# Performance work log

Hardware: AMD Instinct MI355X
Metric: run time of the kernel (lower is better)

Reference implementation:

```python
import jax, jax.numpy as jnp
import numpy as np

N_S, N_T = 64, 32
N_EFF = N_S * N_T          # 2048
K_T1, K_T2 = 8, 8
BATCH = 16


def _orthonormal(key, n):
    q, _ = jnp.linalg.qr(jax.random.normal(key, (n, n), dtype=jnp.float32))
    return q.astype(jnp.float32)


def setup_inputs() -> dict:
    key = jax.random.key(0)
    ks = jax.random.split(key, 6)
    return {
        "s_effective_batch": jax.random.normal(ks[0], (BATCH, N_EFF), dtype=jnp.float32),
        "U_G": _orthonormal(ks[1], N_S),
        "U_P_T": _orthonormal(ks[2], N_T),
        "h0": jax.random.normal(ks[3], (N_EFF,), dtype=jnp.float32) * 0.01,
        "h_hat_1_coeffs": jax.random.normal(ks[4], (N_S, K_T1), dtype=jnp.float32) * 0.01,
        "H_hat_2_S": jax.random.normal(ks[5], (N_S, N_S), dtype=jnp.float32) * 0.01,
        "H_hat_2_T_coeffs": jax.random.normal(jax.random.fold_in(key, 7), (K_T2, K_T2), dtype=jnp.float32) * 0.01,
    }


def reference(s_effective_batch, U_G, U_P_T, h0, h_hat_1_coeffs, H_hat_2_S, H_hat_2_T_coeffs):
    # spatio-temporal basis via Kronecker product: [N_eff, N_eff]
    U_ST = jnp.kron(U_G, U_P_T)

    # GFT as in the module: s_hat = s @ U_ST
    s_hat = s_effective_batch @ U_ST                       # [B, N_eff]

    # linear (first-order Volterra) term
    Ub1 = U_P_T[:, :K_T1]                                  # [N_T, K1]
    full_h_hat_1 = (h_hat_1_coeffs @ Ub1.T).reshape(-1)    # [N_eff]
    z1 = (full_h_hat_1[None, :] * s_hat) @ U_ST            # iGFT as in module: @ U_ST

    # quadratic kernel H2 = kron(H2_S, Ub2 @ C @ Ub2^T)
    Ub2 = U_P_T[:, :K_T2]
    full_H2_T = Ub2 @ (H_hat_2_T_coeffs @ Ub2.T)           # [N_T, N_T]
    H2 = jnp.kron(H_hat_2_S, full_H2_T)                    # [N_eff, N_eff]

    # z2[b,i] = diag( U_ST (H2 * s_hat_b s_hat_b^T) U_ST^T )_i
    #         = sum_{k,l} B[b,i,k] H2[k,l] B[b,i,l], with B[b,i,k] = U_ST[i,k]*s_hat[b,k]
    B = U_ST[None, :, :] * s_hat[:, None, :]               # [B, N_eff, N_eff]
    z2 = jnp.einsum('bik,kl,bil->bi', B, H2, B)            # batched GEMM + row-reduce

    return h0[None, :] + z1 + z2
```

## Files before the change

kernel.cpp:

```cpp
#include <hip/hip_runtime.h>


typedef short  bf16x8 __attribute__((ext_vector_type(8)));
typedef float  f32x4  __attribute__((ext_vector_type(4)));
typedef unsigned short u16;

static __device__ __forceinline__ u16 f2bf(float f) {
  unsigned u = __float_as_uint(f);
  u = (u + 0x7fff + ((u >> 16) & 1)) >> 16;
  return (u16)u;
}
static __device__ __forceinline__ float bf2f(u16 h) {
  return __uint_as_float(((unsigned)h) << 16);
}
static __device__ __forceinline__ float dot4(f32x4 a, f32x4 b) {
  return a.x * b.x + a.y * b.y + a.z * b.z + a.w * b.w;
}

__global__ __launch_bounds__(512) void volterra_one(
    const float* __restrict__ s, const float* __restrict__ UG,
    const float* __restrict__ UPT, const float* __restrict__ h0,
    const float* __restrict__ h1c, const float* __restrict__ HS,
    const float* __restrict__ Hc, float* __restrict__ out)
{
  const int b   = blockIdx.x >> 4;
  const int iT0 = (blockIdx.x & 15) << 1;
  const int t   = threadIdx.x;
  const int w   = t >> 6;
  const int l   = t & 63;
  const int r   = l & 15;
  const int g   = l >> 4;

  __shared__ __align__(16) u16   sSTh[2048], sSTl[2048];
  __shared__ __align__(16) u16   sUGTh[4096], sUGTl[4096];
  __shared__ __align__(16) u16   sUGh[4096];
  __shared__ __align__(16) float sUPT[32][36];
  __shared__ __align__(16) float wGmR[2][288], wAR[2][288], wQR[2][288];
  __shared__ __align__(16) float wGmP[2][288], wAP[2][288], wQP[2][288];
  __shared__ __align__(16) float sT1[64][36];
  __shared__ __align__(16) u16   sGh[2][64][8], sGl[2][64][8];
  __shared__ __align__(16) u16   sAh[2][64][8], sAl[2][64][8];
  __shared__ __align__(16) u16   szero16[8];
  __shared__ __align__(16) u16   sE[2][4096];
  __shared__ float wv[2][64];
  __shared__ float zp1[2][4][64], zpart[2][4][64];

  {
    const f32x4 v = ((const f32x4*)(s + b * 2048))[t];
    const int rr = t >> 3, c0 = (t & 7) * 4;
    const float arr[4] = {v.x, v.y, v.z, v.w};
    #pragma unroll
    for (int i = 0; i < 4; ++i) {
      const int c = c0 + i;
      const u16 hi = f2bf(arr[i]);
      const int ad = c * 64 + (((rr >> 3) ^ (c & 7)) << 3) + (rr & 7);
      sSTh[ad] = hi;
      sSTl[ad] = f2bf(arr[i] - bf2f(hi));
    }
  }
  #pragma unroll
  for (int it = 0; it < 2; ++it) {
    const int o4 = t + it * 512;
    const int rr = o4 >> 4, c0 = (o4 & 15) * 4;
    const f32x4 v = ((const f32x4*)UG)[o4];
    const float arr[4] = {v.x, v.y, v.z, v.w};
    short4 h4;
    h4.x = (short)f2bf(v.x); h4.y = (short)f2bf(v.y);
    h4.z = (short)f2bf(v.z); h4.w = (short)f2bf(v.w);
    *(short4*)&sUGh[rr * 64 + (c0 ^ ((rr & 7) << 3))] = h4;
    #pragma unroll
    for (int i = 0; i < 4; ++i) {
      const int c = c0 + i;
      const u16 hi = f2bf(arr[i]);
      const int ad = c * 64 + (((rr >> 3) ^ (c & 7)) << 3) + (rr & 7);
      sUGTh[ad] = hi;
      sUGTl[ad] = f2bf(arr[i] - bf2f(hi));
    }
  }
  if (t < 256) {
    *(f32x4*)&sUPT[t >> 3][(t & 7) * 4] = ((const f32x4*)UPT)[t];
  }
  if (t < 8) szero16[t] = 0;
  {
    const int side = t >> 8, p = (t >> 5) & 7, k = t & 31;
    const int iTs = iT0 + side;
    const float m1 = UPT[iTs * 32 + k];
    const float m3 = UPT[k * 32 + iTs];
    const float m2 = UPT[k * 32 + p];
    float uh = 0.f;
    #pragma unroll
    for (int q = 0; q < 8; ++q) uh += UPT[k * 32 + q] * Hc[q * 8 + p];
    wGmR[side][p * 36 + k] = m1 * m2;
    wAR [side][p * 36 + k] = m1 * uh;
    wQR [side][p * 36 + k] = m3 * m2;
  }
  __syncthreads();

  {
    const int band = w >> 1, ct = w & 1;
    const int rowA = 16 * band + r, rowB = ct * 16 + r;
    f32x4 acc = {0.f, 0.f, 0.f, 0.f};
    #pragma unroll
    for (int kc = 0; kc < 2; ++kc) {
      const int ch = kc * 4 + g;
      const int oa = rowA * 64 + ((ch ^ (rowA & 7)) << 3);
      const int ob = rowB * 64 + ((ch ^ (rowB & 7)) << 3);
      const bf16x8 Ah = *(const bf16x8*)&sUGTh[oa];
      const bf16x8 Al = *(const bf16x8*)&sUGTl[oa];
      const bf16x8 Bh = *(const bf16x8*)&sSTh[ob];
      const bf16x8 Bl = *(const bf16x8*)&sSTl[ob];
      acc = __builtin_amdgcn_mfma_f32_16x16x32_bf16(Ah, Bh, acc, 0, 0, 0);
      acc = __builtin_amdgcn_mfma_f32_16x16x32_bf16(Ah, Bl, acc, 0, 0, 0);
      acc = __builtin_amdgcn_mfma_f32_16x16x32_bf16(Al, Bh, acc, 0, 0, 0);
    }
    #pragma unroll
    for (int reg = 0; reg < 4; ++reg)
      sT1[16 * band + 4 * g + reg][ct * 16 + r] = acc[reg];
  }
  {
    const int side = t >> 8, p = (t >> 5) & 7, j = t & 31;
    float aG = 0.f, aA = 0.f, aQ = 0.f;
    #pragma unroll
    for (int k4 = 0; k4 < 8; ++k4) {
      const f32x4 u  = *(const f32x4*)&sUPT[j][k4 * 4];
      const f32x4 w1 = *(const f32x4*)&wGmR[side][p * 36 + k4 * 4];
      const f32x4 w2 = *(const f32x4*)&wAR [side][p * 36 + k4 * 4];
      const f32x4 w3 = *(const f32x4*)&wQR [side][p * 36 + k4 * 4];
      aG += dot4(u, w1); aA += dot4(u, w2); aQ += dot4(u, w3);
    }
    wGmP[side][p * 36 + j] = aG;
    wAP [side][p * 36 + j] = aA;
    wQP [side][p * 36 + j] = aQ;
  }
  __syncthreads();

  {
    const int side = t >> 8, ts = t & 255;
    const int kSa = ts >> 3, p = ts & 7;
    float g0 = 0.f, g1v = 0.f, a0 = 0.f, a1v = 0.f, q0 = 0.f, q1v = 0.f;
    #pragma unroll
    for (int c4 = 0; c4 < 8; ++c4) {
      const f32x4 w1 = *(const f32x4*)&wGmP[side][p * 36 + c4 * 4];
      const f32x4 w2 = *(const f32x4*)&wAP [side][p * 36 + c4 * 4];
      const f32x4 w3 = *(const f32x4*)&wQP [side][p * 36 + c4 * 4];
      const f32x4 x0 = *(const f32x4*)&sT1[kSa][c4 * 4];
      const f32x4 x1 = *(const f32x4*)&sT1[kSa + 32][c4 * 4];
      g0  += dot4(x0, w1); a0  += dot4(x0, w2); q0  += dot4(x0, w3);
      g1v += dot4(x1, w1); a1v += dot4(x1, w2); q1v += dot4(x1, w3);
    }
    const u16 gh0 = f2bf(g0);
    sGh[side][kSa][p] = gh0;       sGl[side][kSa][p] = f2bf(g0 - bf2f(gh0));
    const u16 gh1 = f2bf(g1v);
    sGh[side][kSa + 32][p] = gh1;  sGl[side][kSa + 32][p] = f2bf(g1v - bf2f(gh1));
    const u16 ah0 = f2bf(a0);
    sAh[side][kSa][p] = ah0;       sAl[side][kSa][p] = f2bf(a0 - bf2f(ah0));
    const u16 ah1 = f2bf(a1v);
    sAh[side][kSa + 32][p] = ah1;  sAl[side][kSa + 32][p] = f2bf(a1v - bf2f(ah1));
    float wv0 = h1c[kSa * 8 + p] * q0;
    float wv1 = h1c[(kSa + 32) * 8 + p] * q1v;
    wv0 += __shfl_xor(wv0, 1); wv0 += __shfl_xor(wv0, 2); wv0 += __shfl_xor(wv0, 4);
    wv1 += __shfl_xor(wv1, 1); wv1 += __shfl_xor(wv1, 2); wv1 += __shfl_xor(wv1, 4);
    if (p == 0) { wv[side][kSa] = wv0; wv[side][kSa + 32] = wv1; }
  }
  __syncthreads();

  {
    const int side = t >> 8, sub = (t >> 6) & 3;
    const int rowA = 16 * sub + r;
    const u16* ap = (g < 2)  ? &sAh[side][rowA][0]
                  : (g == 2) ? &sAl[side][rowA][0] : szero16;
    const bf16x8 af = *(const bf16x8*)ap;
    #pragma unroll
    for (int cb = 0; cb < 4; ++cb) {
      const int rowB = 16 * cb + r;
      const u16* bp = (g == 0) ? &sGh[side][rowB][0]
                    : (g == 1) ? &sGl[side][rowB][0]
                    : (g == 2) ? &sGh[side][rowB][0] : szero16;
      const bf16x8 bf = *(const bf16x8*)bp;
      f32x4 acc = {0.f, 0.f, 0.f, 0.f};
      acc = __builtin_amdgcn_mfma_f32_16x16x32_bf16(af, bf, acc, 0, 0, 0);
      #pragma unroll
      for (int reg = 0; reg < 4; ++reg) {
        const int row = 16 * sub + 4 * g + reg;
        const int col = 16 * cb + r;
        const float e = acc[reg] * HS[row * 64 + col];
        sE[side][row * 64 + (col ^ ((row & 7) << 3))] = f2bf(e);
      }
    }
    const float wvl = wv[side][l];
    float part = 0.f;
    #pragma unroll
    for (int j = 0; j < 16; ++j) {
      const int kk = 16 * sub + j;
      part += __shfl(wvl, kk) * UG[kk * 64 + l];
    }
    zp1[side][sub][l] = part;
  }
  __syncthreads();

  {
    const int side = t >> 8, sub = (t >> 6) & 3;
    f32x4 acc[4];
    #pragma unroll
    for (int nt = 0; nt < 4; ++nt) acc[nt] = (f32x4){0.f, 0.f, 0.f, 0.f};
    #pragma unroll
    for (int ks = 0; ks < 2; ++ks) {
      const int kcol = g * 8 + ks * 32;
      const int rowA = 16 * sub + r;
      const bf16x8 ah = *(const bf16x8*)&sE[side][rowA * 64 + (kcol ^ ((rowA & 7) << 3))];
      #pragma unroll
      for (int nt = 0; nt < 4; ++nt) {
        const int rowB = 16 * nt + r;
        const bf16x8 bh = *(const bf16x8*)&sUGh[rowB * 64 + (kcol ^ ((rowB & 7) << 3))];
        acc[nt] = __builtin_amdgcn_mfma_f32_16x16x32_bf16(ah, bh, acc[nt], 0, 0, 0);
      }
    }
    #pragma unroll
    for (int nt = 0; nt < 4; ++nt) {
      float zp = 0.f;
      #pragma unroll
      for (int reg = 0; reg < 4; ++reg) {
        const int kS = 16 * sub + 4 * g + reg;
        const int iS = 16 * nt + r;
        zp += bf2f(sUGh[iS * 64 + (kS ^ ((iS & 7) << 3))]) * acc[nt][reg];
      }
      zp += __shfl_xor(zp, 16);
      zp += __shfl_xor(zp, 32);
      if (g == 0) zpart[side][sub][16 * nt + r] = zp;
    }
  }
  __syncthreads();

  if (t < 128) {
    const int side = t >> 6, c = t & 63;
    const float z2 = zpart[side][0][c] + zpart[side][1][c] +
                     zpart[side][2][c] + zpart[side][3][c];
    const float z1 = zp1[side][0][c] + zp1[side][1][c] +
                     zp1[side][2][c] + zp1[side][3][c];
    const int col = c * 32 + iT0 + side;
    out[b * 2048 + col] = h0[col] + z1 + z2;
  }
}

extern "C" void kernel_launch(void* const* d_in, const int* in_sizes, int n_in,
                              void* d_out, int out_size, void* d_ws, size_t ws_size,
                              hipStream_t stream) {
  const float* s   = (const float*)d_in[0];
  const float* UG  = (const float*)d_in[1];
  const float* UPT = (const float*)d_in[2];
  const float* h0  = (const float*)d_in[3];
  const float* h1c = (const float*)d_in[4];
  const float* HS  = (const float*)d_in[5];
  const float* Hc  = (const float*)d_in[6];
  float* out = (float*)d_out;

  volterra_one<<<256, 512, 0, stream>>>(s, UG, UPT, h0, h1c, HS, Hc, out);
}
```

Baseline: 13.35 us.

## Split work to one temporal index per block with 256 threads

Each block now handles a single temporal index iT instead of two, so the launch becomes 512 blocks of 256 threads instead of 256 blocks of 512. Per-side shared arrays collapse to one copy, and the first MFMA stage loops over two column tiles per wave. Because each wave now writes and reads only its own rows of sE, one __syncthreads between the E build and the final GEMM is removed. The aim is more blocks and less shared memory per block for better occupancy and latency hiding, at the cost of doing the per-block staging of s, UG and UPT twice as often.

Result: slower. 14.29 us (+7.1%).

```diff
diff --git a/kernel.cpp b/kernel.cpp
--- a/kernel.cpp
+++ b/kernel.cpp
@@ -17,37 +17,39 @@
   return a.x * b.x + a.y * b.y + a.z * b.z + a.w * b.w;
 }
 
-__global__ __launch_bounds__(512) void volterra_one(
+__global__ __launch_bounds__(256) void volterra_one(
     const float* __restrict__ s, const float* __restrict__ UG,
     const float* __restrict__ UPT, const float* __restrict__ h0,
     const float* __restrict__ h1c, const float* __restrict__ HS,
     const float* __restrict__ Hc, float* __restrict__ out)
 {
-  const int b   = blockIdx.x >> 4;
-  const int iT0 = (blockIdx.x & 15) << 1;
-  const int t   = threadIdx.x;
-  const int w   = t >> 6;
-  const int l   = t & 63;
-  const int r   = l & 15;
-  const int g   = l >> 4;
+  const int b  = blockIdx.x >> 5;
+  const int iT = blockIdx.x & 31;
+  const int t  = threadIdx.x;
+  const int w  = t >> 6;
+  const int l  = t & 63;
+  const int r  = l & 15;
+  const int g  = l >> 4;
 
   __shared__ __align__(16) u16   sSTh[2048], sSTl[2048];
   __shared__ __align__(16) u16   sUGTh[4096], sUGTl[4096];
   __shared__ __align__(16) u16   sUGh[4096];
   __shared__ __align__(16) float sUPT[32][36];
-  __shared__ __align__(16) float wGmR[2][288], wAR[2][288], wQR[2][288];
-  __shared__ __align__(16) float wGmP[2][288], wAP[2][288], wQP[2][288];
+  __shared__ __align__(16) float wGmR[288], wAR[288], wQR[288];
+  __shared__ __align__(16) float wGmP[288], wAP[288], wQP[288];
   __shared__ __align__(16) float sT1[64][36];
-  __shared__ __align__(16) u16   sGh[2][64][8], sGl[2][64][8];
-  __shared__ __align__(16) u16   sAh[2][64][8], sAl[2][64][8];
+  __shared__ __align__(16) u16   sGh[64][8], sGl[64][8];
+  __shared__ __align__(16) u16   sAh[64][8], sAl[64][8];
   __shared__ __align__(16) u16   szero16[8];
-  __shared__ __align__(16) u16   sE[2][4096];
-  __shared__ float wv[2][64];
-  __shared__ float zp1[2][4][64], zpart[2][4][64];
-
-  {
-    const f32x4 v = ((const f32x4*)(s + b * 2048))[t];
-    const int rr = t >> 3, c0 = (t & 7) * 4;
+  __shared__ __align__(16) u16   sE[4096];
+  __shared__ float wv[64];
+  __shared__ float zp1[4][64], zpart[4][64];
+
+  #pragma unroll
+  for (int it = 0; it < 2; ++it) {
+    const int o4 = t + it * 256;
+    const f32x4 v = ((const f32x4*)(s + b * 2048))[o4];
+    const int rr = o4 >> 3, c0 = (o4 & 7) * 4;
     const float arr[4] = {v.x, v.y, v.z, v.w};
     #pragma unroll
     for (int i = 0; i < 4; ++i) {
@@ -59,8 +61,8 @@
     }
   }
   #pragma unroll
-  for (int it = 0; it < 2; ++it) {
-    const int o4 = t + it * 512;
+  for (int it = 0; it < 4; ++it) {
+    const int o4 = t + it * 256;
     const int rr = o4 >> 4, c0 = (o4 & 15) * 4;
     const f32x4 v = ((const f32x4*)UG)[o4];
     const float arr[4] = {v.x, v.y, v.z, v.w};
@@ -77,28 +79,27 @@
       sUGTl[ad] = f2bf(arr[i] - bf2f(hi));
     }
   }
-  if (t < 256) {
+  {
     *(f32x4*)&sUPT[t >> 3][(t & 7) * 4] = ((const f32x4*)UPT)[t];
   }
   if (t < 8) szero16[t] = 0;
   {
-    const int side = t >> 8, p = (t >> 5) & 7, k = t & 31;
-    const int iTs = iT0 + side;
-    const float m1 = UPT[iTs * 32 + k];
-    const float m3 = UPT[k * 32 + iTs];
+    const int p = t >> 5, k = t & 31;
+    const float m1 = UPT[iT * 32 + k];
+    const float m3 = UPT[k * 32 + iT];
     const float m2 = UPT[k * 32 + p];
     float uh = 0.f;
     #pragma unroll
     for (int q = 0; q < 8; ++q) uh += UPT[k * 32 + q] * Hc[q * 8 + p];
-    wGmR[side][p * 36 + k] = m1 * m2;
-    wAR [side][p * 36 + k] = m1 * uh;
-    wQR [side][p * 36 + k] = m3 * m2;
-  }
-  __syncthreads();
-
-  {
-    const int band = w >> 1, ct = w & 1;
-    const int rowA = 16 * band + r, rowB = ct * 16 + r;
+    wGmR[p * 36 + k] = m1 * m2;
+    wAR [p * 36 + k] = m1 * uh;
+    wQR [p * 36 + k] = m3 * m2;
+  }
+  __syncthreads();
+
+  #pragma unroll
+  for (int ct = 0; ct < 2; ++ct) {
+    const int rowA = 16 * w + r, rowB = ct * 16 + r;
     f32x4 acc = {0.f, 0.f, 0.f, 0.f};
     #pragma unroll
     for (int kc = 0; kc < 2; ++kc) {
@@ -115,99 +116,95 @@
     }
     #pragma unroll
     for (int reg = 0; reg < 4; ++reg)
-      sT1[16 * band + 4 * g + reg][ct * 16 + r] = acc[reg];
-  }
-  {
-    const int side = t >> 8, p = (t >> 5) & 7, j = t & 31;
+      sT1[16 * w + 4 * g + reg][ct * 16 + r] = acc[reg];
+  }
+  {
+    const int p = t >> 5, j = t & 31;
     float aG = 0.f, aA = 0.f, aQ = 0.f;
     #pragma unroll
     for (int k4 = 0; k4 < 8; ++k4) {
       const f32x4 u  = *(const f32x4*)&sUPT[j][k4 * 4];
-      const f32x4 w1 = *(const f32x4*)&wGmR[side][p * 36 + k4 * 4];
-      const f32x4 w2 = *(const f32x4*)&wAR [side][p * 36 + k4 * 4];
-      const f32x4 w3 = *(const f32x4*)&wQR [side][p * 36 + k4 * 4];
+      const f32x4 w1 = *(const f32x4*)&wGmR[p * 36 + k4 * 4];
+      const f32x4 w2 = *(const f32x4*)&wAR [p * 36 + k4 * 4];
+      const f32x4 w3 = *(const f32x4*)&wQR [p * 36 + k4 * 4];
       aG += dot4(u, w1); aA += dot4(u, w2); aQ += dot4(u, w3);
     }
-    wGmP[side][p * 36 + j] = aG;
-    wAP [side][p * 36 + j] = aA;
-    wQP [side][p * 36 + j] = aQ;
-  }
-  __syncthreads();
-
-  {
-    const int side = t >> 8, ts = t & 255;
-    const int kSa = ts >> 3, p = ts & 7;
+    wGmP[p * 36 + j] = aG;
+    wAP [p * 36 + j] = aA;
+    wQP [p * 36 + j] = aQ;
+  }
+  __syncthreads();
+
+  {
+    const int kSa = t >> 3, p = t & 7;
     float g0 = 0.f, g1v = 0.f, a0 = 0.f, a1v = 0.f, q0 = 0.f, q1v = 0.f;
     #pragma unroll
     for (int c4 = 0; c4 < 8; ++c4) {
-      const f32x4 w1 = *(const f32x4*)&wGmP[side][p * 36 + c4 * 4];
-      const f32x4 w2 = *(const f32x4*)&wAP [side][p * 36 + c4 * 4];
-      const f32x4 w3 = *(const f32x4*)&wQP [side][p * 36 + c4 * 4];
+      const f32x4 w1 = *(const f32x4*)&wGmP[p * 36 + c4 * 4];
+      const f32x4 w2 = *(const f32x4*)&wAP [p * 36 + c4 * 4];
+      const f32x4 w3 = *(const f32x4*)&wQP [p * 36 + c4 * 4];
       const f32x4 x0 = *(const f32x4*)&sT1[kSa][c4 * 4];
       const f32x4 x1 = *(const f32x4*)&sT1[kSa + 32][c4 * 4];
       g0  += dot4(x0, w1); a0  += dot4(x0, w2); q0  += dot4(x0, w3);
       g1v += dot4(x1, w1); a1v += dot4(x1, w2); q1v += dot4(x1, w3);
     }
     const u16 gh0 = f2bf(g0);
-    sGh[side][kSa][p] = gh0;       sGl[side][kSa][p] = f2bf(g0 - bf2f(gh0));
+    sGh[kSa][p] = gh0;       sGl[kSa][p] = f2bf(g0 - bf2f(gh0));
     const u16 gh1 = f2bf(g1v);
-    sGh[side][kSa + 32][p] = gh1;  sGl[side][kSa + 32][p] = f2bf(g1v - bf2f(gh1));
+    sGh[kSa + 32][p] = gh1;  sGl[kSa + 32][p] = f2bf(g1v - bf2f(gh1));
     const u16 ah0 = f2bf(a0);
-    sAh[side][kSa][p] = ah0;       sAl[side][kSa][p] = f2bf(a0 - bf2f(ah0));
+    sAh[kSa][p] = ah0;       sAl[kSa][p] = f2bf(a0 - bf2f(ah0));
     const u16 ah1 = f2bf(a1v);
-    sAh[side][kSa + 32][p] = ah1;  sAl[side][kSa + 32][p] = f2bf(a1v - bf2f(ah1));
+    sAh[kSa + 32][p] = ah1;  sAl[kSa + 32][p] = f2bf(a1v - bf2f(ah1));
     float wv0 = h1c[kSa * 8 + p] * q0;
     float wv1 = h1c[(kSa + 32) * 8 + p] * q1v;
     wv0 += __shfl_xor(wv0, 1); wv0 += __shfl_xor(wv0, 2); wv0 += __shfl_xor(wv0, 4);
     wv1 += __shfl_xor(wv1, 1); wv1 += __shfl_xor(wv1, 2); wv1 += __shfl_xor(wv1, 4);
-    if (p == 0) { wv[side][kSa] = wv0; wv[side][kSa + 32] = wv1; }
-  }
-  __syncthreads();
-
-  {
-    const int side = t >> 8, sub = (t >> 6) & 3;
-    const int rowA = 16 * sub + r;
-    const u16* ap = (g < 2)  ? &sAh[side][rowA][0]
-                  : (g == 2) ? &sAl[side][rowA][0] : szero16;
+    if (p == 0) { wv[kSa] = wv0; wv[kSa + 32] = wv1; }
+  }
+  __syncthreads();
+
+  {
+    const int rowA = 16 * w + r;
+    const u16* ap = (g < 2)  ? &sAh[rowA][0]
+                  : (g == 2) ? &sAl[rowA][0] : szero16;
     const bf16x8 af = *(const bf16x8*)ap;
     #pragma unroll
     for (int cb = 0; cb < 4; ++cb) {
       const int rowB = 16 * cb + r;
-      const u16* bp = (g == 0) ? &sGh[side][rowB][0]
-                    : (g == 1) ? &sGl[side][rowB][0]
-                    : (g == 2) ? &sGh[side][rowB][0] : szero16;
+      const u16* bp = (g == 0) ? &sGh[rowB][0]
+                    : (g == 1) ? &sGl[rowB][0]
+                    : (g == 2) ? &sGh[rowB][0] : szero16;
       const bf16x8 bf = *(const bf16x8*)bp;
       f32x4 acc = {0.f, 0.f, 0.f, 0.f};
       acc = __builtin_amdgcn_mfma_f32_16x16x32_bf16(af, bf, acc, 0, 0, 0);
       #pragma unroll
       for (int reg = 0; reg < 4; ++reg) {
-        const int row = 16 * sub + 4 * g + reg;
+        const int row = 16 * w + 4 * g + reg;
         const int col = 16 * cb + r;
         const float e = acc[reg] * HS[row * 64 + col];
-        sE[side][row * 64 + (col ^ ((row & 7) << 3))] = f2bf(e);
+        sE[row * 64 + (col ^ ((row & 7) << 3))] = f2bf(e);
       }
     }
-    const float wvl = wv[side][l];
+    const float wvl = wv[l];
     float part = 0.f;
     #pragma unroll
     for (int j = 0; j < 16; ++j) {
-      const int kk = 16 * sub + j;
+      const int kk = 16 * w + j;
       part += __shfl(wvl, kk) * UG[kk * 64 + l];
     }
-    zp1[side][sub][l] = part;
-  }
-  __syncthreads();
-
-  {
-    const int side = t >> 8, sub = (t >> 6) & 3;
+    zp1[w][l] = part;
+  }
+
+  {
     f32x4 acc[4];
     #pragma unroll
     for (int nt = 0; nt < 4; ++nt) acc[nt] = (f32x4){0.f, 0.f, 0.f, 0.f};
     #pragma unroll
     for (int ks = 0; ks < 2; ++ks) {
       const int kcol = g * 8 + ks * 32;
-      const int rowA = 16 * sub + r;
-      const bf16x8 ah = *(const bf16x8*)&sE[side][rowA * 64 + (kcol ^ ((rowA & 7) << 3))];
+      const int rowA = 16 * w + r;
+      const bf16x8 ah = *(const bf16x8*)&sE[rowA * 64 + (kcol ^ ((rowA & 7) << 3))];
       #pragma unroll
       for (int nt = 0; nt < 4; ++nt) {
         const int rowB = 16 * nt + r;
@@ -220,24 +217,21 @@
       float zp = 0.f;
       #pragma unroll
       for (int reg = 0; reg < 4; ++reg) {
-        const int kS = 16 * sub + 4 * g + reg;
+        const int kS = 16 * w + 4 * g + reg;
         const int iS = 16 * nt + r;
         zp += bf2f(sUGh[iS * 64 + (kS ^ ((iS & 7) << 3))]) * acc[nt][reg];
       }
       zp += __shfl_xor(zp, 16);
       zp += __shfl_xor(zp, 32);
-      if (g == 0) zpart[side][sub][16 * nt + r] = zp;
-    }
-  }
-  __syncthreads();
-
-  if (t < 128) {
-    const int side = t >> 6, c = t & 63;
-    const float z2 = zpart[side][0][c] + zpart[side][1][c] +
-                     zpart[side][2][c] + zpart[side][3][c];
-    const float z1 = zp1[side][0][c] + zp1[side][1][c] +
-                     zp1[side][2][c] + zp1[side][3][c];
-    const int col = c * 32 + iT0 + side;
+      if (g == 0) zpart[w][16 * nt + r] = zp;
+    }
+  }
+  __syncthreads();
+
+  if (t < 64) {
+    const float z2 = zpart[0][t] + zpart[1][t] + zpart[2][t] + zpart[3][t];
+    const float z1 = zp1[0][t] + zp1[1][t] + zp1[2][t] + zp1[3][t];
+    const int col = t * 32 + iT;
     out[b * 2048 + col] = h0[col] + z1 + z2;
   }
 }
@@ -254,5 +248,5 @@
   const float* Hc  = (const float*)d_in[6];
   float* out = (float*)d_out;
 
-  volterra_one<<<256, 512, 0, stream>>>(s, UG, UPT, h0, h1c, HS, Hc, out);
-}
+  volterra_one<<<512, 256, 0, stream>>>(s, UG, UPT, h0, h1c, HS, Hc, out);
+}
```

## Replace scalar FP32 projection stage with split-bf16 MFMA and drop a barrier

Applied to the files above, without the earlier changes.

The intermediate T1 and the temporal projection weights are now stored as hi/lo bf16 pairs in swizzled shared memory. The G/A/Q projections are computed with 16x16x32 MFMA in three-term split precision instead of per-thread FP32 dot-product loops, and the separate wGmP/wAP/wQP staging buffers are removed. The h1c weighted reduction moves into the MFMA epilogue through shuffles. One __syncthreads before the sE GEMM stage is also removed, which relies on each wave reading only the sE rows it wrote itself. The split-bf16 scheme keeps close to FP32 accuracy but adds conversion work, and zero padding is used for the unused Q half.

New measurement: 12.97 us. 2.8% less time.

```diff
diff --git a/kernel.cpp b/kernel.cpp
--- a/kernel.cpp
+++ b/kernel.cpp
@@ -15,6 +15,11 @@
 }
 static __device__ __forceinline__ float dot4(f32x4 a, f32x4 b) {
   return a.x * b.x + a.y * b.y + a.z * b.z + a.w * b.w;
+}
+static __device__ __forceinline__ int padr(int row, int col) {
+  return row * 32 +
+         ((((col >> 3) ^ (row & 3) ^ (((row >> 2) & 1) << 1)) & 3) << 3) +
+         (col & 7);
 }
 
 __global__ __launch_bounds__(512) void volterra_one(
@@ -36,8 +41,9 @@
   __shared__ __align__(16) u16   sUGh[4096];
   __shared__ __align__(16) float sUPT[32][36];
   __shared__ __align__(16) float wGmR[2][288], wAR[2][288], wQR[2][288];
-  __shared__ __align__(16) float wGmP[2][288], wAP[2][288], wQP[2][288];
-  __shared__ __align__(16) float sT1[64][36];
+  __shared__ __align__(16) u16   sT1h[2048], sT1l[2048];
+  __shared__ __align__(16) u16   sWGAh[2][512], sWGAl[2][512];
+  __shared__ __align__(16) u16   sWQh[2][512], sWQl[2][512];
   __shared__ __align__(16) u16   sGh[2][64][8], sGl[2][64][8];
   __shared__ __align__(16) u16   sAh[2][64][8], sAl[2][64][8];
   __shared__ __align__(16) u16   szero16[8];
@@ -114,8 +120,13 @@
       acc = __builtin_amdgcn_mfma_f32_16x16x32_bf16(Al, Bh, acc, 0, 0, 0);
     }
     #pragma unroll
-    for (int reg = 0; reg < 4; ++reg)
-      sT1[16 * band + 4 * g + reg][ct * 16 + r] = acc[reg];
+    for (int reg = 0; reg < 4; ++reg) {
+      const int row = 16 * band + 4 * g + reg;
+      const int ad = padr(row, ct * 16 + r);
+      const u16 hi = f2bf(acc[reg]);
+      sT1h[ad] = hi;
+      sT1l[ad] = f2bf(acc[reg] - bf2f(hi));
+    }
   }
   {
     const int side = t >> 8, p = (t >> 5) & 7, j = t & 31;
@@ -128,39 +139,47 @@
       const f32x4 w3 = *(const f32x4*)&wQR [side][p * 36 + k4 * 4];
       aG += dot4(u, w1); aA += dot4(u, w2); aQ += dot4(u, w3);
     }
-    wGmP[side][p * 36 + j] = aG;
-    wAP [side][p * 36 + j] = aA;
-    wQP [side][p * 36 + j] = aQ;
-  }
-  __syncthreads();
-
-  {
-    const int side = t >> 8, ts = t & 255;
-    const int kSa = ts >> 3, p = ts & 7;
-    float g0 = 0.f, g1v = 0.f, a0 = 0.f, a1v = 0.f, q0 = 0.f, q1v = 0.f;
-    #pragma unroll
-    for (int c4 = 0; c4 < 8; ++c4) {
-      const f32x4 w1 = *(const f32x4*)&wGmP[side][p * 36 + c4 * 4];
-      const f32x4 w2 = *(const f32x4*)&wAP [side][p * 36 + c4 * 4];
-      const f32x4 w3 = *(const f32x4*)&wQP [side][p * 36 + c4 * 4];
-      const f32x4 x0 = *(const f32x4*)&sT1[kSa][c4 * 4];
-      const f32x4 x1 = *(const f32x4*)&sT1[kSa + 32][c4 * 4];
-      g0  += dot4(x0, w1); a0  += dot4(x0, w2); q0  += dot4(x0, w3);
-      g1v += dot4(x1, w1); a1v += dot4(x1, w2); q1v += dot4(x1, w3);
-    }
-    const u16 gh0 = f2bf(g0);
-    sGh[side][kSa][p] = gh0;       sGl[side][kSa][p] = f2bf(g0 - bf2f(gh0));
-    const u16 gh1 = f2bf(g1v);
-    sGh[side][kSa + 32][p] = gh1;  sGl[side][kSa + 32][p] = f2bf(g1v - bf2f(gh1));
-    const u16 ah0 = f2bf(a0);
-    sAh[side][kSa][p] = ah0;       sAl[side][kSa][p] = f2bf(a0 - bf2f(ah0));
-    const u16 ah1 = f2bf(a1v);
-    sAh[side][kSa + 32][p] = ah1;  sAl[side][kSa + 32][p] = f2bf(a1v - bf2f(ah1));
-    float wv0 = h1c[kSa * 8 + p] * q0;
-    float wv1 = h1c[(kSa + 32) * 8 + p] * q1v;
-    wv0 += __shfl_xor(wv0, 1); wv0 += __shfl_xor(wv0, 2); wv0 += __shfl_xor(wv0, 4);
-    wv1 += __shfl_xor(wv1, 1); wv1 += __shfl_xor(wv1, 2); wv1 += __shfl_xor(wv1, 4);
-    if (p == 0) { wv[side][kSa] = wv0; wv[side][kSa + 32] = wv1; }
+    const int adG = padr(p, j), adA = padr(8 + p, j);
+    u16 h;
+    h = f2bf(aG); sWGAh[side][adG] = h; sWGAl[side][adG] = f2bf(aG - bf2f(h));
+    h = f2bf(aA); sWGAh[side][adA] = h; sWGAl[side][adA] = f2bf(aA - bf2f(h));
+    h = f2bf(aQ); sWQh[side][adG]  = h; sWQl[side][adG]  = f2bf(aQ - bf2f(h));
+    sWQh[side][adA] = 0; sWQl[side][adA] = 0;
+  }
+  __syncthreads();
+
+  {
+    const int side = t >> 8, sub = (t >> 6) & 3;
+    const int rowA = 16 * sub + r;
+    const int oa = padr(rowA, g * 8);
+    const bf16x8 Ah = *(const bf16x8*)&sT1h[oa];
+    const bf16x8 Al = *(const bf16x8*)&sT1l[oa];
+    const int ob = padr(r, g * 8);
+    const bf16x8 GAh = *(const bf16x8*)&sWGAh[side][ob];
+    const bf16x8 GAl = *(const bf16x8*)&sWGAl[side][ob];
+    const bf16x8 Qh  = *(const bf16x8*)&sWQh[side][ob];
+    const bf16x8 Ql  = *(const bf16x8*)&sWQl[side][ob];
+    f32x4 accGA = {0.f, 0.f, 0.f, 0.f}, accQ = {0.f, 0.f, 0.f, 0.f};
+    accGA = __builtin_amdgcn_mfma_f32_16x16x32_bf16(Ah, GAh, accGA, 0, 0, 0);
+    accGA = __builtin_amdgcn_mfma_f32_16x16x32_bf16(Ah, GAl, accGA, 0, 0, 0);
+    accGA = __builtin_amdgcn_mfma_f32_16x16x32_bf16(Al, GAh, accGA, 0, 0, 0);
+    accQ  = __builtin_amdgcn_mfma_f32_16x16x32_bf16(Ah, Qh,  accQ,  0, 0, 0);
+    accQ  = __builtin_amdgcn_mfma_f32_16x16x32_bf16(Ah, Ql,  accQ,  0, 0, 0);
+    accQ  = __builtin_amdgcn_mfma_f32_16x16x32_bf16(Al, Qh,  accQ,  0, 0, 0);
+    #pragma unroll
+    for (int reg = 0; reg < 4; ++reg) {
+      const int row = 16 * sub + 4 * g + reg;
+      const float v = accGA[reg];
+      const u16 h = f2bf(v);
+      const u16 lo = f2bf(v - bf2f(h));
+      if (r < 8) { sGh[side][row][r] = h;     sGl[side][row][r] = lo; }
+      else       { sAh[side][row][r - 8] = h; sAl[side][row][r - 8] = lo; }
+      float pr = (r < 8) ? h1c[row * 8 + r] * accQ[reg] : 0.f;
+      pr += __shfl_xor(pr, 1);
+      pr += __shfl_xor(pr, 2);
+      pr += __shfl_xor(pr, 4);
+      if (r == 0) wv[side][row] = pr;
+    }
   }
   __syncthreads();
 
@@ -196,7 +215,6 @@
     }
     zp1[side][sub][l] = part;
   }
-  __syncthreads();
 
   {
     const int side = t >> 8, sub = (t >> 6) & 3;
```
